# Performance work log

Measured on AMD Instinct MI355X. Metric: run time of the kernel, lower is better.

## Reference

```python
import jax, jax.numpy as jnp
import numpy as np
import math

D_MODEL, D_K, D_V = 1024, 64, 64
B, S = 4, 4096


def setup_inputs() -> dict:
    key = jax.random.key(0)
    ks = jax.random.split(key, 7)
    lim = 1.0 / math.sqrt(D_MODEL)
    return {
        "embeddings": jax.random.normal(ks[0], (B, S, D_MODEL), dtype=jnp.float32),
        "Wq": jax.random.uniform(ks[1], (D_MODEL, D_K), minval=-lim, maxval=lim, dtype=jnp.float32),
        "bq": jax.random.uniform(ks[2], (D_K,), minval=-lim, maxval=lim, dtype=jnp.float32),
        "Wk": jax.random.uniform(ks[3], (D_MODEL, D_K), minval=-lim, maxval=lim, dtype=jnp.float32),
        "bk": jax.random.uniform(ks[4], (D_K,), minval=-lim, maxval=lim, dtype=jnp.float32),
        "Wv": jax.random.uniform(ks[5], (D_MODEL, D_V), minval=-lim, maxval=lim, dtype=jnp.float32),
        "bv": jax.random.uniform(ks[6], (D_V,), minval=-lim, maxval=lim, dtype=jnp.float32),
    }


def reference(embeddings, Wq, bq, Wk, bk, Wv, bv):
    # Q, K: [B, S, d_k]; V: [B, S, d_v]
    Q = embeddings @ Wq + bq
    K = embeddings @ Wk + bk
    V = embeddings @ Wv + bv
    scale = 1.0 / math.sqrt(D_K)
    # scores: [B, S, S]
    scores = jnp.einsum("bsk,btk->bst", Q, K) * scale
    attn = jax.nn.softmax(scores, axis=-1)
    return jnp.einsum("bst,btv->bsv", attn, V)
```

## Files before the change

kernel.cpp:

```cpp
#include <hip/hip_runtime.h>

#define SEQ  4096
#define DMODEL 1024
#define QTOT 16384
#define NQK (QTOT * 128)
#define NV  (QTOT * 64)
#define QSCALE 0.18033688011112042f

typedef __bf16 bf16x8 __attribute__((ext_vector_type(8)));
typedef unsigned short u16x8 __attribute__((ext_vector_type(8)));
typedef float f32x4 __attribute__((ext_vector_type(4)));

static __device__ __forceinline__ unsigned short f2bfbits(float f) {
    unsigned int u = __builtin_bit_cast(unsigned int, f);
    unsigned int lsb = (u >> 16) & 1u;
    u += 0x7fffu + lsb;
    return (unsigned short)(u >> 16);
}

static __device__ __forceinline__ bf16x8 ld_frag(const unsigned short* p) {
    uint4 u = *reinterpret_cast<const uint4*>(p);
    return __builtin_bit_cast(bf16x8, u);
}

static __device__ __forceinline__ void stp(float* p, float v) { *p = v; }
static __device__ __forceinline__ void stp(unsigned short* p, float v) { *p = f2bfbits(v); }

__global__ void prep_weights(const float* __restrict__ Wq,
                             const float* __restrict__ Wk,
                             const float* __restrict__ Wv,
                             unsigned short* __restrict__ WtS) {
    int o = blockIdx.x * 256 + threadIdx.x;
    int f = o >> 9, q = o & 511;
    int lane = q >> 3, j = q & 7;
    int kc = f / 12, nt = f - kc * 12;
    int n = nt * 16 + (lane & 15);
    int k = kc * 32 + (lane >> 4) * 8 + j;
    float v;
    if (n < 64)       v = Wq[k * 64 + n];
    else if (n < 128) v = Wk[k * 64 + (n - 64)];
    else              v = Wv[k * 64 + (n - 128)];
    WtS[o] = f2bfbits(v);
}

template <typename T>
__global__ __launch_bounds__(256) void proj_split(
        const float* __restrict__ emb, const unsigned short* __restrict__ WtS,
        T* __restrict__ PQK, T* __restrict__ PV) {
    const int tid = threadIdx.x;
    const int w = tid >> 6, lane = tid & 63;
    const int c = lane & 15, qd = lane >> 4;
    const int split = blockIdx.x >> 8;
    const int tb = blockIdx.x & 255;
    const int mbase = tb * 64 + w * 16;
    const int kbase = split * 512;

    f32x4 acc[12];
#pragma unroll
    for (int i = 0; i < 12; i++) acc[i] = (f32x4){0.f, 0.f, 0.f, 0.f};

    const float* ap = emb + (size_t)(mbase + c) * DMODEL + kbase + qd * 8;
    const unsigned short* wp = WtS + (size_t)(kbase >> 5) * 6144 + lane * 8;

    float4 e0a = *reinterpret_cast<const float4*>(ap);
    float4 e0b = *reinterpret_cast<const float4*>(ap + 4);
    float4 e1a = *reinterpret_cast<const float4*>(ap + 32);
    float4 e1b = *reinterpret_cast<const float4*>(ap + 36);
    bf16x8 wc[12];
#pragma unroll
    for (int nt = 0; nt < 12; nt++) wc[nt] = ld_frag(wp + nt * 512);

#pragma unroll
    for (int s = 0; s < 16; s++) {
        bf16x8 wn[12];
        if (s < 15) {
#pragma unroll
            for (int nt = 0; nt < 12; nt++)
                wn[nt] = ld_frag(wp + (s + 1) * 6144 + nt * 512);
        } else {
#pragma unroll
            for (int nt = 0; nt < 12; nt++) wn[nt] = wc[nt];
        }
        float4 e2a, e2b;
        if (s < 14) {
            e2a = *reinterpret_cast<const float4*>(ap + (s + 2) * 32);
            e2b = *reinterpret_cast<const float4*>(ap + (s + 2) * 32 + 4);
        } else { e2a = e1a; e2b = e1b; }

        u16x8 at;
        at[0] = f2bfbits(e0a.x); at[1] = f2bfbits(e0a.y);
        at[2] = f2bfbits(e0a.z); at[3] = f2bfbits(e0a.w);
        at[4] = f2bfbits(e0b.x); at[5] = f2bfbits(e0b.y);
        at[6] = f2bfbits(e0b.z); at[7] = f2bfbits(e0b.w);
        bf16x8 af = __builtin_bit_cast(bf16x8, at);

#pragma unroll
        for (int nt = 0; nt < 12; nt++)
            acc[nt] = __builtin_amdgcn_mfma_f32_16x16x32_bf16(af, wc[nt], acc[nt], 0, 0, 0);

        e0a = e1a; e0b = e1b; e1a = e2a; e1b = e2b;
#pragma unroll
        for (int nt = 0; nt < 12; nt++) wc[nt] = wn[nt];
    }

#pragma unroll
    for (int nt = 0; nt < 12; nt++) {
        int n = nt * 16 + c;
#pragma unroll
        for (int r = 0; r < 4; r++) {
            int token = mbase + qd * 4 + r;
            if (n < 128)
                stp(&PQK[(size_t)split * NQK + (size_t)token * 128 + n], acc[nt][r]);
            else {
                int bb = token >> 12, s = token & 4095, v = n - 128;
                stp(&PV[(size_t)split * NV + ((size_t)bb << 18) + (v << 12) + s], acc[nt][r]);
            }
        }
    }
}

template <typename T>
__global__ __launch_bounds__(256) void merge_proj(
        const T* __restrict__ PQK, const T* __restrict__ PV,
        const float* __restrict__ bq, const float* __restrict__ bk,
        const float* __restrict__ bv,
        unsigned short* __restrict__ Qb, unsigned short* __restrict__ Kb,
        unsigned short* __restrict__ VT) {
    int idx4 = (blockIdx.x * 256 + threadIdx.x) * 4;
    float s[4];
    if (idx4 < NQK) {
        int token = idx4 >> 7, n = idx4 & 127;
#pragma unroll
        for (int j = 0; j < 4; j++) s[j] = 0.f;
#pragma unroll
        for (int kz = 0; kz < 2; kz++) {
            if constexpr (sizeof(T) == 4) {
                float4 v = *reinterpret_cast<const float4*>(&PQK[(size_t)kz * NQK + idx4]);
                s[0] += v.x; s[1] += v.y; s[2] += v.z; s[3] += v.w;
            } else {
                ushort4 v = *reinterpret_cast<const ushort4*>(&PQK[(size_t)kz * NQK + idx4]);
                s[0] += __builtin_bit_cast(float, (unsigned int)v.x << 16);
                s[1] += __builtin_bit_cast(float, (unsigned int)v.y << 16);
                s[2] += __builtin_bit_cast(float, (unsigned int)v.z << 16);
                s[3] += __builtin_bit_cast(float, (unsigned int)v.w << 16);
            }
        }
        bool isQ = (n < 64);
        const float* bias = isQ ? bq + n : bk + (n - 64);
        float fac = isQ ? QSCALE : 1.0f;
        unsigned short* dst = isQ ? Qb + (size_t)token * 64 + n
                                  : Kb + (size_t)token * 64 + (n - 64);
#pragma unroll
        for (int j = 0; j < 4; j++) dst[j] = f2bfbits((s[j] + bias[j]) * fac);
    } else {
        int j0 = idx4 - NQK;
        int v = (j0 >> 12) & 63;
        float bias = bv[v];
#pragma unroll
        for (int j = 0; j < 4; j++) s[j] = bias;
#pragma unroll
        for (int kz = 0; kz < 2; kz++) {
            if constexpr (sizeof(T) == 4) {
                float4 vv = *reinterpret_cast<const float4*>(&PV[(size_t)kz * NV + j0]);
                s[0] += vv.x; s[1] += vv.y; s[2] += vv.z; s[3] += vv.w;
            } else {
                ushort4 vv = *reinterpret_cast<const ushort4*>(&PV[(size_t)kz * NV + j0]);
                s[0] += __builtin_bit_cast(float, (unsigned int)vv.x << 16);
                s[1] += __builtin_bit_cast(float, (unsigned int)vv.y << 16);
                s[2] += __builtin_bit_cast(float, (unsigned int)vv.z << 16);
                s[3] += __builtin_bit_cast(float, (unsigned int)vv.w << 16);
            }
        }
#pragma unroll
        for (int j = 0; j < 4; j++) VT[j0 + j] = f2bfbits(s[j]);
    }
}

__global__ __launch_bounds__(256) void proj_direct(
        const float* __restrict__ emb, const unsigned short* __restrict__ WtS,
        const float* __restrict__ bq, const float* __restrict__ bk,
        const float* __restrict__ bv,
        unsigned short* __restrict__ Qb, unsigned short* __restrict__ Kb,
        unsigned short* __restrict__ VT) {
    const int tid = threadIdx.x;
    const int w = tid >> 6, lane = tid & 63;
    const int c = lane & 15, qd = lane >> 4;
    const int mbase = blockIdx.x * 64 + w * 16;

    f32x4 acc[12];
#pragma unroll
    for (int i = 0; i < 12; i++) acc[i] = (f32x4){0.f, 0.f, 0.f, 0.f};

    const float* ap = emb + (size_t)(mbase + c) * DMODEL + qd * 8;
    const unsigned short* wp = WtS + lane * 8;

    float4 e0a = *reinterpret_cast<const float4*>(ap);
    float4 e0b = *reinterpret_cast<const float4*>(ap + 4);
    float4 e1a = *reinterpret_cast<const float4*>(ap + 32);
    float4 e1b = *reinterpret_cast<const float4*>(ap + 36);
    bf16x8 wc[12];
#pragma unroll
    for (int nt = 0; nt < 12; nt++) wc[nt] = ld_frag(wp + nt * 512);

#pragma unroll 4
    for (int s = 0; s < 32; s++) {
        bf16x8 wn[12];
        if (s < 31) {
#pragma unroll
            for (int nt = 0; nt < 12; nt++)
                wn[nt] = ld_frag(wp + (s + 1) * 6144 + nt * 512);
        } else {
#pragma unroll
            for (int nt = 0; nt < 12; nt++) wn[nt] = wc[nt];
        }
        float4 e2a, e2b;
        if (s < 30) {
            e2a = *reinterpret_cast<const float4*>(ap + (s + 2) * 32);
            e2b = *reinterpret_cast<const float4*>(ap + (s + 2) * 32 + 4);
        } else { e2a = e1a; e2b = e1b; }

        u16x8 at;
        at[0] = f2bfbits(e0a.x); at[1] = f2bfbits(e0a.y);
        at[2] = f2bfbits(e0a.z); at[3] = f2bfbits(e0a.w);
        at[4] = f2bfbits(e0b.x); at[5] = f2bfbits(e0b.y);
        at[6] = f2bfbits(e0b.z); at[7] = f2bfbits(e0b.w);
        bf16x8 af = __builtin_bit_cast(bf16x8, at);

#pragma unroll
        for (int nt = 0; nt < 12; nt++)
            acc[nt] = __builtin_amdgcn_mfma_f32_16x16x32_bf16(af, wc[nt], acc[nt], 0, 0, 0);

        e0a = e1a; e0b = e1b; e1a = e2a; e1b = e2b;
#pragma unroll
        for (int nt = 0; nt < 12; nt++) wc[nt] = wn[nt];
    }

#pragma unroll
    for (int nt = 0; nt < 12; nt++) {
        int n = nt * 16 + c;
        float bias = (n < 64) ? bq[n] : (n < 128) ? bk[n - 64] : bv[n - 128];
        float fac = (n < 64) ? QSCALE : 1.0f;
#pragma unroll
        for (int r = 0; r < 4; r++) {
            int token = mbase + qd * 4 + r;
            unsigned short bits = f2bfbits((acc[nt][r] + bias) * fac);
            if (n < 64)        Qb[(size_t)token * 64 + n] = bits;
            else if (n < 128)  Kb[(size_t)token * 64 + (n - 64)] = bits;
            else {
                int bb = token >> 12, ss = token & 4095;
                VT[((size_t)bb * 64 + (n - 128)) * SEQ + ss] = bits;
            }
        }
    }
}

__global__ __launch_bounds__(512, 2) void attn(
        const unsigned short* __restrict__ Qb, const unsigned short* __restrict__ Kb,
        const unsigned short* __restrict__ VT, float* __restrict__ out) {
    __shared__ __align__(16) unsigned short Pl[8][64 * 72];
    __shared__ float l_all[8][64];

    const int tid = threadIdx.x;
    const int w = tid >> 6, lane = tid & 63;
    const int c = lane & 15, qd = lane >> 4;
    const int g3 = blockIdx.x & 7;
    const int b = g3 >> 1;
    const int qblk = ((blockIdx.x >> 3) << 1) | (g3 & 1);
    const int qbase = qblk * 64;
    const int tstart = w * 512;

    bf16x8 aq0[4], aq1[4];
#pragma unroll
    for (int qs = 0; qs < 4; qs++) {
        const unsigned short* Qp = Qb + ((size_t)(b << 12) + qbase + qs * 16 + c) * 64 + qd * 8;
        aq0[qs] = ld_frag(Qp);
        aq1[qs] = ld_frag(Qp + 32);
    }

    f32x4 acc[16];
#pragma unroll
    for (int i = 0; i < 16; i++) acc[i] = (f32x4){0.f, 0.f, 0.f, 0.f};
    float lsum[4][4];
#pragma unroll
    for (int qs = 0; qs < 4; qs++)
#pragma unroll
        for (int r = 0; r < 4; r++) lsum[qs][r] = 0.f;

    unsigned short* myP = &Pl[w][0];

#pragma unroll 2
    for (int it = 0; it < 8; it++) {
        const int t0 = tstart + it * 64;
        const unsigned short* Kt = Kb + ((size_t)(b << 12) + t0) * 64;

        bf16x8 bk0[4], bk1[4];
#pragma unroll
        for (int ts = 0; ts < 4; ts++) {
            bk0[ts] = ld_frag(Kt + (ts * 16 + c) * 64 + qd * 8);
            bk1[ts] = ld_frag(Kt + (ts * 16 + c) * 64 + 32 + qd * 8);
        }

#pragma unroll
        for (int qs = 0; qs < 4; qs++) {
            f32x4 sc[4];
#pragma unroll
            for (int ts = 0; ts < 4; ts++) {
                f32x4 z = (f32x4){0.f, 0.f, 0.f, 0.f};
                z = __builtin_amdgcn_mfma_f32_16x16x32_bf16(aq0[qs], bk0[ts], z, 0, 0, 0);
                z = __builtin_amdgcn_mfma_f32_16x16x32_bf16(aq1[qs], bk1[ts], z, 0, 0, 0);
                sc[ts] = z;
            }
#pragma unroll
            for (int ts = 0; ts < 4; ts++)
#pragma unroll
                for (int r = 0; r < 4; r++) {
                    float p = __builtin_amdgcn_exp2f(sc[ts][r]);
                    lsum[qs][r] += p;
                    myP[(qs * 16 + qd * 4 + r) * 72 + ts * 16 + c] = f2bfbits(p);
                }
        }

        bf16x8 bv0[4], bv1[4];
#pragma unroll
        for (int nt = 0; nt < 4; nt++) {
            const unsigned short* Vp = VT + (((size_t)b * 64 + nt * 16 + c) << 12) + t0 + qd * 8;
            bv0[nt] = ld_frag(Vp);
            bv1[nt] = ld_frag(Vp + 32);
        }

#pragma unroll
        for (int qs = 0; qs < 4; qs++) {
            bf16x8 ap0 = ld_frag(&myP[(qs * 16 + c) * 72 + qd * 8]);
            bf16x8 ap1 = ld_frag(&myP[(qs * 16 + c) * 72 + 32 + qd * 8]);
#pragma unroll
            for (int nt = 0; nt < 4; nt++) {
                acc[qs * 4 + nt] = __builtin_amdgcn_mfma_f32_16x16x32_bf16(ap0, bv0[nt], acc[qs * 4 + nt], 0, 0, 0);
                acc[qs * 4 + nt] = __builtin_amdgcn_mfma_f32_16x16x32_bf16(ap1, bv1[nt], acc[qs * 4 + nt], 0, 0, 0);
            }
        }
    }

#pragma unroll
    for (int off = 1; off < 16; off <<= 1)
#pragma unroll
        for (int qs = 0; qs < 4; qs++)
#pragma unroll
            for (int r = 0; r < 4; r++) lsum[qs][r] += __shfl_xor(lsum[qs][r], off);
    if (c == 0) {
#pragma unroll
        for (int qs = 0; qs < 4; qs++)
#pragma unroll
            for (int r = 0; r < 4; r++)
                l_all[w][qs * 16 + qd * 4 + r] = lsum[qs][r];
    }

    float* red = (float*)&Pl[0][0];
    __syncthreads();
    if (w >= 4) {
        float* rp = red + (w - 4) * 4352 + lane * 68;
#pragma unroll
        for (int i = 0; i < 16; i++) *reinterpret_cast<f32x4*>(rp + i * 4) = acc[i];
    }
    __syncthreads();
    if (w < 4) {
        float* rp = red + w * 4352 + lane * 68;
#pragma unroll
        for (int i = 0; i < 16; i++) acc[i] += *reinterpret_cast<const f32x4*>(rp + i * 4);
    }
    __syncthreads();
    if (w == 2 || w == 3) {
        float* rp = red + (w - 2) * 4352 + lane * 68;
#pragma unroll
        for (int i = 0; i < 16; i++) *reinterpret_cast<f32x4*>(rp + i * 4) = acc[i];
    }
    __syncthreads();
    if (w < 2) {
        float* rp = red + w * 4352 + lane * 68;
#pragma unroll
        for (int i = 0; i < 16; i++) acc[i] += *reinterpret_cast<const f32x4*>(rp + i * 4);
    }
    __syncthreads();
    if (w == 1) {
        float* rp = red + lane * 68;
#pragma unroll
        for (int i = 0; i < 16; i++) *reinterpret_cast<f32x4*>(rp + i * 4) = acc[i];
    }
    __syncthreads();
    if (w == 0) {
        float* rp = red + lane * 68;
#pragma unroll
        for (int i = 0; i < 16; i++) acc[i] += *reinterpret_cast<const f32x4*>(rp + i * 4);
#pragma unroll
        for (int qs = 0; qs < 4; qs++)
#pragma unroll
            for (int r = 0; r < 4; r++) {
                int q = qs * 16 + qd * 4 + r;
                float l = 0.f;
#pragma unroll
                for (int ww = 0; ww < 8; ww++) l += l_all[ww][q];
                float inv = 1.0f / l;
                size_t row = (size_t)(b << 12) + qbase + q;
#pragma unroll
                for (int nt = 0; nt < 4; nt++)
                    out[row * 64 + nt * 16 + c] = acc[qs * 4 + nt][r] * inv;
            }
    }
}

extern "C" void kernel_launch(void* const* d_in, const int* in_sizes, int n_in,
                              void* d_out, int out_size, void* d_ws, size_t ws_size,
                              hipStream_t stream) {
    const float* emb = (const float*)d_in[0];
    const float* Wq  = (const float*)d_in[1];
    const float* bq  = (const float*)d_in[2];
    const float* Wk  = (const float*)d_in[3];
    const float* bk  = (const float*)d_in[4];
    const float* Wv  = (const float*)d_in[5];
    const float* bv  = (const float*)d_in[6];
    float* out = (float*)d_out;

    unsigned short* ws = (unsigned short*)d_ws;
    unsigned short* WtS = ws;
    unsigned short* Qb = ws + 192 * 1024;
    unsigned short* Kb = Qb + QTOT * 64;
    unsigned short* VT = Kb + QTOT * 64;
    char* region = (char*)(VT + QTOT * 64);
    size_t avail = (ws_size > 6684672) ? ws_size - 6684672 : 0;

    int projMode = (avail >= (size_t)2 * (NQK + NV) * 4) ? 2
                 : (avail >= (size_t)2 * (NQK + NV) * 2) ? 1 : 0;

    prep_weights<<<768, 256, 0, stream>>>(Wq, Wk, Wv, WtS);

    if (projMode == 2) {
        float* PQKp = (float*)region;
        float* PVp  = PQKp + (size_t)2 * NQK;
        proj_split<float><<<512, 256, 0, stream>>>(emb, WtS, PQKp, PVp);
        merge_proj<float><<<3072, 256, 0, stream>>>(PQKp, PVp, bq, bk, bv, Qb, Kb, VT);
    } else if (projMode == 1) {
        unsigned short* PQKp = (unsigned short*)region;
        unsigned short* PVp  = PQKp + (size_t)2 * NQK;
        proj_split<unsigned short><<<512, 256, 0, stream>>>(emb, WtS, PQKp, PVp);
        merge_proj<unsigned short><<<3072, 256, 0, stream>>>(PQKp, PVp, bq, bk, bv, Qb, Kb, VT);
    } else {
        proj_direct<<<256, 256, 0, stream>>>(emb, WtS, bq, bk, bv, Qb, Kb, VT);
    }

    attn<<<256, 512, 0, stream>>>(Qb, Kb, VT, out);
}
```

Before: 172.0 us.

## Fuse split-K projection and merge into one kernel with LDS reduction

```diff
diff --git a/kernel.cpp b/kernel.cpp
--- a/kernel.cpp
+++ b/kernel.cpp
@@ -3,8 +3,6 @@
 #define SEQ  4096
 #define DMODEL 1024
 #define QTOT 16384
-#define NQK (QTOT * 128)
-#define NV  (QTOT * 64)
 #define QSCALE 0.18033688011112042f
 
 typedef __bf16 bf16x8 __attribute__((ext_vector_type(8)));
@@ -22,9 +20,6 @@
     uint4 u = *reinterpret_cast<const uint4*>(p);
     return __builtin_bit_cast(bf16x8, u);
 }
-
-static __device__ __forceinline__ void stp(float* p, float v) { *p = v; }
-static __device__ __forceinline__ void stp(unsigned short* p, float v) { *p = f2bfbits(v); }
 
 __global__ void prep_weights(const float* __restrict__ Wq,
                              const float* __restrict__ Wk,
@@ -43,17 +38,20 @@
     WtS[o] = f2bfbits(v);
 }
 
-template <typename T>
-__global__ __launch_bounds__(256) void proj_split(
+__global__ __launch_bounds__(512, 2) void proj_fused(
         const float* __restrict__ emb, const unsigned short* __restrict__ WtS,
-        T* __restrict__ PQK, T* __restrict__ PV) {
+        const float* __restrict__ bq, const float* __restrict__ bk,
+        const float* __restrict__ bv,
+        unsigned short* __restrict__ Qb, unsigned short* __restrict__ Kb,
+        unsigned short* __restrict__ VT) {
+    __shared__ __align__(16) float red[2][3][16][196];
+
     const int tid = threadIdx.x;
     const int w = tid >> 6, lane = tid & 63;
     const int c = lane & 15, qd = lane >> 4;
-    const int split = blockIdx.x >> 8;
-    const int tb = blockIdx.x & 255;
-    const int mbase = tb * 64 + w * 16;
-    const int kbase = split * 512;
+    const int m = w & 1, kz = w >> 1;
+    const int mbase = blockIdx.x * 32 + m * 16;
+    const int kbase = kz * 256;
 
     f32x4 acc[12];
 #pragma unroll
@@ -71,9 +69,9 @@
     for (int nt = 0; nt < 12; nt++) wc[nt] = ld_frag(wp + nt * 512);
 
 #pragma unroll
-    for (int s = 0; s < 16; s++) {
+    for (int s = 0; s < 8; s++) {
         bf16x8 wn[12];
-        if (s < 15) {
+        if (s < 7) {
 #pragma unroll
             for (int nt = 0; nt < 12; nt++)
                 wn[nt] = ld_frag(wp + (s + 1) * 6144 + nt * 512);
@@ -82,7 +80,7 @@
             for (int nt = 0; nt < 12; nt++) wn[nt] = wc[nt];
         }
         float4 e2a, e2b;
-        if (s < 14) {
+        if (s < 6) {
             e2a = *reinterpret_cast<const float4*>(ap + (s + 2) * 32);
             e2b = *reinterpret_cast<const float4*>(ap + (s + 2) * 32 + 4);
         } else { e2a = e1a; e2b = e1b; }
@@ -103,152 +101,35 @@
         for (int nt = 0; nt < 12; nt++) wc[nt] = wn[nt];
     }
 
-#pragma unroll
-    for (int nt = 0; nt < 12; nt++) {
-        int n = nt * 16 + c;
-#pragma unroll
-        for (int r = 0; r < 4; r++) {
-            int token = mbase + qd * 4 + r;
-            if (n < 128)
-                stp(&PQK[(size_t)split * NQK + (size_t)token * 128 + n], acc[nt][r]);
-            else {
-                int bb = token >> 12, s = token & 4095, v = n - 128;
-                stp(&PV[(size_t)split * NV + ((size_t)bb << 18) + (v << 12) + s], acc[nt][r]);
-            }
-        }
-    }
-}
-
-template <typename T>
-__global__ __launch_bounds__(256) void merge_proj(
-        const T* __restrict__ PQK, const T* __restrict__ PV,
-        const float* __restrict__ bq, const float* __restrict__ bk,
-        const float* __restrict__ bv,
-        unsigned short* __restrict__ Qb, unsigned short* __restrict__ Kb,
-        unsigned short* __restrict__ VT) {
-    int idx4 = (blockIdx.x * 256 + threadIdx.x) * 4;
-    float s[4];
-    if (idx4 < NQK) {
-        int token = idx4 >> 7, n = idx4 & 127;
-#pragma unroll
-        for (int j = 0; j < 4; j++) s[j] = 0.f;
-#pragma unroll
-        for (int kz = 0; kz < 2; kz++) {
-            if constexpr (sizeof(T) == 4) {
-                float4 v = *reinterpret_cast<const float4*>(&PQK[(size_t)kz * NQK + idx4]);
-                s[0] += v.x; s[1] += v.y; s[2] += v.z; s[3] += v.w;
-            } else {
-                ushort4 v = *reinterpret_cast<const ushort4*>(&PQK[(size_t)kz * NQK + idx4]);
-                s[0] += __builtin_bit_cast(float, (unsigned int)v.x << 16);
-                s[1] += __builtin_bit_cast(float, (unsigned int)v.y << 16);
-                s[2] += __builtin_bit_cast(float, (unsigned int)v.z << 16);
-                s[3] += __builtin_bit_cast(float, (unsigned int)v.w << 16);
-            }
-        }
-        bool isQ = (n < 64);
-        const float* bias = isQ ? bq + n : bk + (n - 64);
-        float fac = isQ ? QSCALE : 1.0f;
-        unsigned short* dst = isQ ? Qb + (size_t)token * 64 + n
-                                  : Kb + (size_t)token * 64 + (n - 64);
-#pragma unroll
-        for (int j = 0; j < 4; j++) dst[j] = f2bfbits((s[j] + bias[j]) * fac);
-    } else {
-        int j0 = idx4 - NQK;
-        int v = (j0 >> 12) & 63;
-        float bias = bv[v];
-#pragma unroll
-        for (int j = 0; j < 4; j++) s[j] = bias;
-#pragma unroll
-        for (int kz = 0; kz < 2; kz++) {
-            if constexpr (sizeof(T) == 4) {
-                float4 vv = *reinterpret_cast<const float4*>(&PV[(size_t)kz * NV + j0]);
-                s[0] += vv.x; s[1] += vv.y; s[2] += vv.z; s[3] += vv.w;
-            } else {
-                ushort4 vv = *reinterpret_cast<const ushort4*>(&PV[(size_t)kz * NV + j0]);
-                s[0] += __builtin_bit_cast(float, (unsigned int)vv.x << 16);
-                s[1] += __builtin_bit_cast(float, (unsigned int)vv.y << 16);
-                s[2] += __builtin_bit_cast(float, (unsigned int)vv.z << 16);
-                s[3] += __builtin_bit_cast(float, (unsigned int)vv.w << 16);
-            }
-        }
-#pragma unroll
-        for (int j = 0; j < 4; j++) VT[j0 + j] = f2bfbits(s[j]);
-    }
-}
-
-__global__ __launch_bounds__(256) void proj_direct(
-        const float* __restrict__ emb, const unsigned short* __restrict__ WtS,
-        const float* __restrict__ bq, const float* __restrict__ bk,
-        const float* __restrict__ bv,
-        unsigned short* __restrict__ Qb, unsigned short* __restrict__ Kb,
-        unsigned short* __restrict__ VT) {
-    const int tid = threadIdx.x;
-    const int w = tid >> 6, lane = tid & 63;
-    const int c = lane & 15, qd = lane >> 4;
-    const int mbase = blockIdx.x * 64 + w * 16;
-
-    f32x4 acc[12];
-#pragma unroll
-    for (int i = 0; i < 12; i++) acc[i] = (f32x4){0.f, 0.f, 0.f, 0.f};
-
-    const float* ap = emb + (size_t)(mbase + c) * DMODEL + qd * 8;
-    const unsigned short* wp = WtS + lane * 8;
-
-    float4 e0a = *reinterpret_cast<const float4*>(ap);
-    float4 e0b = *reinterpret_cast<const float4*>(ap + 4);
-    float4 e1a = *reinterpret_cast<const float4*>(ap + 32);
-    float4 e1b = *reinterpret_cast<const float4*>(ap + 36);
-    bf16x8 wc[12];
-#pragma unroll
-    for (int nt = 0; nt < 12; nt++) wc[nt] = ld_frag(wp + nt * 512);
-
-#pragma unroll 4
-    for (int s = 0; s < 32; s++) {
-        bf16x8 wn[12];
-        if (s < 31) {
-#pragma unroll
-            for (int nt = 0; nt < 12; nt++)
-                wn[nt] = ld_frag(wp + (s + 1) * 6144 + nt * 512);
-        } else {
-#pragma unroll
-            for (int nt = 0; nt < 12; nt++) wn[nt] = wc[nt];
-        }
-        float4 e2a, e2b;
-        if (s < 30) {
-            e2a = *reinterpret_cast<const float4*>(ap + (s + 2) * 32);
-            e2b = *reinterpret_cast<const float4*>(ap + (s + 2) * 32 + 4);
-        } else { e2a = e1a; e2b = e1b; }
-
-        u16x8 at;
-        at[0] = f2bfbits(e0a.x); at[1] = f2bfbits(e0a.y);
-        at[2] = f2bfbits(e0a.z); at[3] = f2bfbits(e0a.w);
-        at[4] = f2bfbits(e0b.x); at[5] = f2bfbits(e0b.y);
-        at[6] = f2bfbits(e0b.z); at[7] = f2bfbits(e0b.w);
-        bf16x8 af = __builtin_bit_cast(bf16x8, at);
-
+    if (kz > 0) {
 #pragma unroll
         for (int nt = 0; nt < 12; nt++)
-            acc[nt] = __builtin_amdgcn_mfma_f32_16x16x32_bf16(af, wc[nt], acc[nt], 0, 0, 0);
-
-        e0a = e1a; e0b = e1b; e1a = e2a; e1b = e2b;
-#pragma unroll
-        for (int nt = 0; nt < 12; nt++) wc[nt] = wn[nt];
-    }
-
-#pragma unroll
-    for (int nt = 0; nt < 12; nt++) {
-        int n = nt * 16 + c;
-        float bias = (n < 64) ? bq[n] : (n < 128) ? bk[n - 64] : bv[n - 128];
-        float fac = (n < 64) ? QSCALE : 1.0f;
-#pragma unroll
-        for (int r = 0; r < 4; r++) {
-            int token = mbase + qd * 4 + r;
-            unsigned short bits = f2bfbits((acc[nt][r] + bias) * fac);
-            if (n < 64)        Qb[(size_t)token * 64 + n] = bits;
-            else if (n < 128)  Kb[(size_t)token * 64 + (n - 64)] = bits;
-            else {
-                int bb = token >> 12, ss = token & 4095;
-                VT[((size_t)bb * 64 + (n - 128)) * SEQ + ss] = bits;
+#pragma unroll
+            for (int r = 0; r < 4; r++)
+                red[m][kz - 1][qd * 4 + r][nt * 16 + c] = acc[nt][r];
+    }
+    __syncthreads();
+    if (kz == 0) {
+#pragma unroll
+        for (int nt = 0; nt < 12; nt++) {
+            int n = nt * 16 + c;
+            float bias = (n < 64) ? bq[n] : (n < 128) ? bk[n - 64] : bv[n - 128];
+            float fac = (n < 64) ? QSCALE : 1.0f;
+#pragma unroll
+            for (int r = 0; r < 4; r++) {
+                int row = qd * 4 + r;
+                float v = acc[nt][r]
+                        + red[m][0][row][n]
+                        + red[m][1][row][n]
+                        + red[m][2][row][n];
+                int token = mbase + row;
+                unsigned short bits = f2bfbits((v + bias) * fac);
+                if (n < 64)        Qb[(size_t)token * 64 + n] = bits;
+                else if (n < 128)  Kb[(size_t)token * 64 + (n - 64)] = bits;
+                else {
+                    int bb = token >> 12, ss = token & 4095;
+                    VT[((size_t)bb * 64 + (n - 128)) * SEQ + ss] = bits;
+                }
             }
         }
     }
@@ -424,27 +305,8 @@
     unsigned short* Qb = ws + 192 * 1024;
     unsigned short* Kb = Qb + QTOT * 64;
     unsigned short* VT = Kb + QTOT * 64;
-    char* region = (char*)(VT + QTOT * 64);
-    size_t avail = (ws_size > 6684672) ? ws_size - 6684672 : 0;
-
-    int projMode = (avail >= (size_t)2 * (NQK + NV) * 4) ? 2
-                 : (avail >= (size_t)2 * (NQK + NV) * 2) ? 1 : 0;
 
     prep_weights<<<768, 256, 0, stream>>>(Wq, Wk, Wv, WtS);
-
-    if (projMode == 2) {
-        float* PQKp = (float*)region;
-        float* PVp  = PQKp + (size_t)2 * NQK;
-        proj_split<float><<<512, 256, 0, stream>>>(emb, WtS, PQKp, PVp);
-        merge_proj<float><<<3072, 256, 0, stream>>>(PQKp, PVp, bq, bk, bv, Qb, Kb, VT);
-    } else if (projMode == 1) {
-        unsigned short* PQKp = (unsigned short*)region;
-        unsigned short* PVp  = PQKp + (size_t)2 * NQK;
-        proj_split<unsigned short><<<512, 256, 0, stream>>>(emb, WtS, PQKp, PVp);
-        merge_proj<unsigned short><<<3072, 256, 0, stream>>>(PQKp, PVp, bq, bk, bv, Qb, Kb, VT);
-    } else {
-        proj_direct<<<256, 256, 0, stream>>>(emb, WtS, bq, bk, bv, Qb, Kb, VT);
-    }
-
+    proj_fused<<<512, 512, 0, stream>>>(emb, WtS, bq, bk, bv, Qb, Kb, VT);
     attn<<<256, 512, 0, stream>>>(Qb, Kb, VT, out);
 }
```

Result: faster. 162.5 us (-5.5%).
